# Optimization experiments

Measured on AMD Instinct MI355X. Metric: run time of the kernel, lower is better.

## Reference

```python
import jax, jax.numpy as jnp
import numpy as np

INPUT, HIDDEN, OUT = 512, 512, 1

def setup_inputs() -> dict:
    key = jax.random.key(0)
    ks = jax.random.split(key, 7)
    B, T = 64, 1024
    s_x = 1.0 / np.sqrt(INPUT)
    s_h = 1.0 / np.sqrt(HIDDEN)
    return {
        "x": jax.random.normal(ks[0], (B, T, INPUT), dtype=jnp.float32),
        "W_x": jax.random.uniform(ks[1], (INPUT, HIDDEN), jnp.float32, -s_x, s_x),
        "b_x": jax.random.uniform(ks[2], (HIDDEN,), jnp.float32, -s_x, s_x),
        "W_h": jax.random.uniform(ks[3], (HIDDEN, HIDDEN), jnp.float32, -s_h, s_h),
        "b_h": jax.random.uniform(ks[4], (HIDDEN,), jnp.float32, -s_h, s_h),
        "W_fc": jax.random.uniform(ks[5], (HIDDEN, OUT), jnp.float32, -s_h, s_h),
        "b_fc": jax.random.uniform(ks[6], (OUT,), jnp.float32, -s_h, s_h),
    }

def reference(x, W_x, b_x, W_h, b_h, W_fc, b_fc):
    # Inference mode: dropout is identity (nn.Dropout in eval).
    B = x.shape[0]
    # Precompute input projections for all timesteps in one GEMM: [B,T,H]
    xw = jnp.einsum('bti,ih->bth', x, W_x) + b_x + b_h
    h0 = jnp.zeros((B, HIDDEN), dtype=x.dtype)
    def step(h, xw_t):
        h = jnp.tanh(xw_t + h @ W_h)
        return h, None
    h_T, _ = jax.lax.scan(step, h0, jnp.swapaxes(xw, 0, 1))  # scan over T
    return h_T @ W_fc + b_fc
```

## Files before the change

kernel.cpp:

```cpp
#include <hip/hip_runtime.h>
#include <hip/hip_bf16.h>


#define T_STEPS 1024
#define HID     512

typedef __attribute__((ext_vector_type(8))) short  short8;
typedef __attribute__((ext_vector_type(4))) short  short4_t;
typedef __attribute__((ext_vector_type(4))) float  f32x4;

typedef unsigned short ushort_t;
typedef unsigned int   uint_t;

__device__ __forceinline__ ushort_t f2bf(float f) {
    union { float f; uint_t u; } c; c.f = f;
    uint_t u = c.u;
    return (ushort_t)((u + 0x7fffu + ((u >> 16) & 1u)) >> 16);
}
__device__ __forceinline__ float bf2f(ushort_t h) {
    union { uint_t u; float f; } c; c.u = ((uint_t)h) << 16;
    return c.f;
}
__device__ __forceinline__ float tanh_fast(float x) {
    float t = __builtin_amdgcn_exp2f(x * 2.88539008f);
    return 1.0f - 2.0f * __builtin_amdgcn_rcpf(t + 1.0f);
}

__global__ __launch_bounds__(256) void k1_xproj(
    const float* __restrict__ x, const float* __restrict__ Wx,
    const float* __restrict__ bx, const float* __restrict__ bh,
    ushort_t* __restrict__ xw)
{
    __shared__ __align__(16) ushort_t Wl[64 * 40];
    __shared__ __align__(16) ushort_t Xl[4][64 * 40];

    const int t0   = blockIdx.y * 4;
    const int n0   = blockIdx.x * 64;
    const int tid  = threadIdx.x;
    const int wave = tid >> 6;
    const int lane = tid & 63;
    const int lm   = lane & 15;
    const int quad = lane >> 4;

    f32x4 acc[4][4];
    #pragma unroll
    for (int tt = 0; tt < 4; ++tt)
        #pragma unroll
        for (int i = 0; i < 4; ++i) acc[tt][i] = (f32x4){0.f, 0.f, 0.f, 0.f};

    float biasv[4];
    #pragma unroll
    for (int r = 0; r < 4; ++r) {
        int n = n0 + wave * 16 + quad * 4 + r;
        biasv[r] = bx[n] + bh[n];
    }

    const int ar = tid >> 2, ac = (tid & 3) * 8;
    const int bk = tid >> 3, bc = (tid & 7) * 8;

    for (int kb = 0; kb < 16; ++kb) {
        {
            const float* bp = Wx + (size_t)(kb * 32 + bk) * HID + n0 + bc;
            #pragma unroll
            for (int i = 0; i < 8; ++i) Wl[(bc + i) * 40 + bk] = f2bf(bp[i]);
        }
        #pragma unroll
        for (int tt = 0; tt < 4; ++tt) {
            const float* ap = x + ((size_t)ar * T_STEPS + t0 + tt) * HID + kb * 32 + ac;
            short8 pack;
            #pragma unroll
            for (int i = 0; i < 8; ++i) pack[i] = (short)f2bf(ap[i]);
            *(short8*)&Xl[tt][ar * 40 + ac] = pack;
        }
        __syncthreads();
        short8 afr = *(const short8*)&Wl[(wave * 16 + lm) * 40 + quad * 8];
        #pragma unroll
        for (int tt = 0; tt < 4; ++tt)
            #pragma unroll
            for (int bt = 0; bt < 4; ++bt) {
                short8 bfr = *(const short8*)&Xl[tt][(bt * 16 + lm) * 40 + quad * 8];
                acc[tt][bt] = __builtin_amdgcn_mfma_f32_16x16x32_bf16(afr, bfr, acc[tt][bt], 0, 0, 0);
            }
        __syncthreads();
    }

    #pragma unroll
    for (int tt = 0; tt < 4; ++tt)
        #pragma unroll
        for (int bt = 0; bt < 4; ++bt) {
            short4_t pk;
            #pragma unroll
            for (int r = 0; r < 4; ++r) pk[r] = (short)f2bf(acc[tt][bt][r] + biasv[r]);
            *(short4_t*)&xw[((size_t)(t0 + tt) * 64 + bt * 16 + lm) * HID
                            + n0 + wave * 16 + quad * 4] = pk;
        }
}

__global__ __launch_bounds__(512, 2) void k2_scan(
    const ushort_t* __restrict__ xw, const float* __restrict__ Wh,
    const float* __restrict__ Wfc, const float* __restrict__ bfc,
    float* __restrict__ out)
{
    __shared__ __align__(16) ushort_t hT[2][8192];
    __shared__ __align__(16) ushort_t Wl[49152];

    const int tid  = threadIdx.x;
    const int wave = tid >> 6;
    const int lane = tid & 63;
    const int lm   = lane & 15;
    const int quad = lane >> 4;
    const int rowbase = blockIdx.x * 16;
    const int colb    = wave * 64;

    for (int i = tid; i < 8192; i += 512) hT[0][i] = 0;

    for (int i = 0; i < 12; ++i) {
        int c   = i * 512 + tid;
        int l   = c & 63;
        int mtg = (c >> 6) & 31;
        int ktp = c >> 11;
        int n   = mtg * 16 + (l & 15);
        int kb  = (13 + ktp) * 32 + (l >> 4) * 8;
        short8 w;
        #pragma unroll
        for (int j = 0; j < 8; ++j) w[j] = (short)f2bf(Wh[(size_t)(kb + j) * HID + n]);
        *(short8*)&Wl[(size_t)c * 8] = w;
    }

    short8 wfA[4][13];
    #pragma unroll
    for (int mt = 0; mt < 4; ++mt) {
        const int n = colb + mt * 16 + lm;
        #pragma unroll
        for (int kt = 0; kt < 13; ++kt) {
            short8 w;
            #pragma unroll
            for (int j = 0; j < 8; ++j)
                w[j] = (short)f2bf(Wh[(size_t)(kt * 32 + quad * 8 + j) * HID + n]);
            wfA[mt][kt] = w;
        }
    }
    __syncthreads();

    for (int t = 0; t < T_STEPS; ++t) {
        short4_t xv[4];
        #pragma unroll
        for (int mt = 0; mt < 4; ++mt)
            xv[mt] = *(const short4_t*)&xw[((size_t)t * 64 + rowbase + lm) * HID
                                           + colb + mt * 16 + quad * 4];

        f32x4 acc[4];
        #pragma unroll
        for (int mt = 0; mt < 4; ++mt) acc[mt] = (f32x4){0.f, 0.f, 0.f, 0.f};

        const ushort_t* cur = hT[t & 1];
        #pragma unroll
        for (int kt = 0; kt < 13; ++kt) {
            short8 b = *(const short8*)&cur[(kt * 64 + lane) * 8];
            #pragma unroll
            for (int mt = 0; mt < 4; ++mt)
                acc[mt] = __builtin_amdgcn_mfma_f32_16x16x32_bf16(wfA[mt][kt], b, acc[mt], 0, 0, 0);
        }
        #pragma unroll
        for (int ktp = 0; ktp < 3; ++ktp) {
            short8 b = *(const short8*)&cur[((13 + ktp) * 64 + lane) * 8];
            #pragma unroll
            for (int mt = 0; mt < 4; ++mt) {
                short8 a = *(const short8*)&Wl[(size_t)((ktp * 32 + wave * 4 + mt) * 64 + lane) * 8];
                acc[mt] = __builtin_amdgcn_mfma_f32_16x16x32_bf16(a, b, acc[mt], 0, 0, 0);
            }
        }

        ushort_t* nxt = hT[(t + 1) & 1];
        #pragma unroll
        for (int mt = 0; mt < 4; ++mt) {
            float v0 = tanh_fast(acc[mt][0] + bf2f((ushort_t)xv[mt][0]));
            float v1 = tanh_fast(acc[mt][1] + bf2f((ushort_t)xv[mt][1]));
            float v2 = tanh_fast(acc[mt][2] + bf2f((ushort_t)xv[mt][2]));
            float v3 = tanh_fast(acc[mt][3] + bf2f((ushort_t)xv[mt][3]));
            union { short4_t v; __hip_bfloat162 h[2]; } cv;
            cv.h[0] = __float22bfloat162_rn(float2{v0, v1});
            cv.h[1] = __float22bfloat162_rn(float2{v2, v3});
            const int n = colb + mt * 16 + quad * 4;
            *(short4_t*)&nxt[((n >> 5) * 64 + ((n >> 3) & 3) * 16 + lm) * 8 + (n & 7)] = cv.v;
        }

        __syncthreads();
    }

    const ushort_t* fin = hT[T_STEPS & 1];
    #pragma unroll
    for (int bb = 0; bb < 2; ++bb) {
        const int b = wave * 2 + bb;
        short8 hv = *(const short8*)&fin[(((lane >> 2) * 64 + (lane & 3) * 16 + b) * 8)];
        float s = 0.f;
        #pragma unroll
        for (int j = 0; j < 8; ++j) s += bf2f((ushort_t)hv[j]) * Wfc[lane * 8 + j];
        #pragma unroll
        for (int off = 32; off; off >>= 1) s += __shfl_down(s, off, 64);
        if (lane == 0) out[rowbase + b] = s + bfc[0];
    }
}

extern "C" void kernel_launch(void* const* d_in, const int* in_sizes, int n_in,
                              void* d_out, int out_size, void* d_ws, size_t ws_size,
                              hipStream_t stream)
{
    const float* x   = (const float*)d_in[0];
    const float* Wx  = (const float*)d_in[1];
    const float* bx  = (const float*)d_in[2];
    const float* Wh  = (const float*)d_in[3];
    const float* bh  = (const float*)d_in[4];
    const float* Wfc = (const float*)d_in[5];
    const float* bfc = (const float*)d_in[6];
    float* out = (float*)d_out;

    ushort_t* xw = (ushort_t*)d_ws;

    k1_xproj<<<dim3(8, 256), 256, 0, stream>>>(x, Wx, bx, bh, xw);
    k2_scan <<<dim3(4),      512, 0, stream>>>(xw, Wh, Wfc, bfc, out);
}
```

Baseline: 2.772 ms.

## Widen xproj tiles to 256 columns and shift Wh split toward LDS

The input-projection kernel now uses 512-thread blocks covering 256 output columns and 4 timesteps, so each x tile is loaded and converted once for four times as many columns, and x is read with float4 loads. In the scan kernel, one more K-tile of W_h moves from registers to LDS (12 register tiles instead of 13, 4 LDS tiles instead of 3), which frees VGPRs at the cost of extra LDS reads per step. The xw pointer is also strength-reduced across timesteps. Risks include higher register pressure in k1 (32 accumulators plus 8 A fragments) and more LDS traffic on the serial scan's critical path.

```diff
diff --git a/kernel.cpp b/kernel.cpp
--- a/kernel.cpp
+++ b/kernel.cpp
@@ -8,6 +8,7 @@
 typedef __attribute__((ext_vector_type(8))) short  short8;
 typedef __attribute__((ext_vector_type(4))) short  short4_t;
 typedef __attribute__((ext_vector_type(4))) float  f32x4;
+typedef __attribute__((ext_vector_type(4))) float  float4_t;
 
 typedef unsigned short ushort_t;
 typedef unsigned int   uint_t;
@@ -26,74 +27,80 @@
     return 1.0f - 2.0f * __builtin_amdgcn_rcpf(t + 1.0f);
 }
 
-__global__ __launch_bounds__(256) void k1_xproj(
+__global__ __launch_bounds__(512) void k1_xproj(
     const float* __restrict__ x, const float* __restrict__ Wx,
     const float* __restrict__ bx, const float* __restrict__ bh,
     ushort_t* __restrict__ xw)
 {
-    __shared__ __align__(16) ushort_t Wl[64 * 40];
+    __shared__ __align__(16) ushort_t Wl[256 * 40];
     __shared__ __align__(16) ushort_t Xl[4][64 * 40];
 
-    const int t0   = blockIdx.y * 4;
-    const int n0   = blockIdx.x * 64;
-    const int tid  = threadIdx.x;
-    const int wave = tid >> 6;
-    const int lane = tid & 63;
-    const int lm   = lane & 15;
-    const int quad = lane >> 4;
-
-    f32x4 acc[4][4];
-    #pragma unroll
-    for (int tt = 0; tt < 4; ++tt)
-        #pragma unroll
-        for (int i = 0; i < 4; ++i) acc[tt][i] = (f32x4){0.f, 0.f, 0.f, 0.f};
-
-    float biasv[4];
-    #pragma unroll
-    for (int r = 0; r < 4; ++r) {
-        int n = n0 + wave * 16 + quad * 4 + r;
-        biasv[r] = bx[n] + bh[n];
-    }
-
-    const int ar = tid >> 2, ac = (tid & 3) * 8;
-    const int bk = tid >> 3, bc = (tid & 7) * 8;
+    const int n0    = blockIdx.x * 256;
+    const int t0    = blockIdx.y * 4;
+    const int tid   = threadIdx.x;
+    const int wave  = tid >> 6;
+    const int lane  = tid & 63;
+    const int lm    = lane & 15;
+    const int quad  = lane >> 4;
+    const int t_loc = wave & 3;
+    const int nsub  = (wave >> 2) * 128;
+
+    f32x4 acc[8][4];
+    #pragma unroll
+    for (int mt = 0; mt < 8; ++mt)
+        #pragma unroll
+        for (int bt = 0; bt < 4; ++bt) acc[mt][bt] = (f32x4){0.f, 0.f, 0.f, 0.f};
+
+    const int wk = tid >> 4, wc = (tid & 15) * 16;
+    const int xb = tid >> 3, xc = (tid & 7) * 4;
 
     for (int kb = 0; kb < 16; ++kb) {
         {
-            const float* bp = Wx + (size_t)(kb * 32 + bk) * HID + n0 + bc;
-            #pragma unroll
-            for (int i = 0; i < 8; ++i) Wl[(bc + i) * 40 + bk] = f2bf(bp[i]);
+            const float* wp = Wx + (size_t)(kb * 32 + wk) * HID + n0 + wc;
+            #pragma unroll
+            for (int j = 0; j < 16; ++j) Wl[(wc + j) * 40 + wk] = f2bf(wp[j]);
         }
         #pragma unroll
         for (int tt = 0; tt < 4; ++tt) {
-            const float* ap = x + ((size_t)ar * T_STEPS + t0 + tt) * HID + kb * 32 + ac;
-            short8 pack;
-            #pragma unroll
-            for (int i = 0; i < 8; ++i) pack[i] = (short)f2bf(ap[i]);
-            *(short8*)&Xl[tt][ar * 40 + ac] = pack;
+            const float* ap = x + ((size_t)xb * T_STEPS + t0 + tt) * HID + kb * 32 + xc;
+            float4_t v = *(const float4_t*)ap;
+            short4_t pk;
+            #pragma unroll
+            for (int j = 0; j < 4; ++j) pk[j] = (short)f2bf(v[j]);
+            *(short4_t*)&Xl[tt][xb * 40 + xc] = pk;
         }
         __syncthreads();
-        short8 afr = *(const short8*)&Wl[(wave * 16 + lm) * 40 + quad * 8];
-        #pragma unroll
-        for (int tt = 0; tt < 4; ++tt)
-            #pragma unroll
-            for (int bt = 0; bt < 4; ++bt) {
-                short8 bfr = *(const short8*)&Xl[tt][(bt * 16 + lm) * 40 + quad * 8];
-                acc[tt][bt] = __builtin_amdgcn_mfma_f32_16x16x32_bf16(afr, bfr, acc[tt][bt], 0, 0, 0);
-            }
+        short8 afr[8];
+        #pragma unroll
+        for (int mt = 0; mt < 8; ++mt)
+            afr[mt] = *(const short8*)&Wl[(nsub + mt * 16 + lm) * 40 + quad * 8];
+        #pragma unroll
+        for (int bt = 0; bt < 4; ++bt) {
+            short8 bfr = *(const short8*)&Xl[t_loc][(bt * 16 + lm) * 40 + quad * 8];
+            #pragma unroll
+            for (int mt = 0; mt < 8; ++mt)
+                acc[mt][bt] = __builtin_amdgcn_mfma_f32_16x16x32_bf16(afr[mt], bfr, acc[mt][bt], 0, 0, 0);
+        }
         __syncthreads();
     }
 
     #pragma unroll
-    for (int tt = 0; tt < 4; ++tt)
+    for (int mt = 0; mt < 8; ++mt) {
+        float biasv[4];
+        #pragma unroll
+        for (int r = 0; r < 4; ++r) {
+            int n = n0 + nsub + mt * 16 + quad * 4 + r;
+            biasv[r] = bx[n] + bh[n];
+        }
         #pragma unroll
         for (int bt = 0; bt < 4; ++bt) {
             short4_t pk;
             #pragma unroll
-            for (int r = 0; r < 4; ++r) pk[r] = (short)f2bf(acc[tt][bt][r] + biasv[r]);
-            *(short4_t*)&xw[((size_t)(t0 + tt) * 64 + bt * 16 + lm) * HID
-                            + n0 + wave * 16 + quad * 4] = pk;
-        }
+            for (int r = 0; r < 4; ++r) pk[r] = (short)f2bf(acc[mt][bt][r] + biasv[r]);
+            *(short4_t*)&xw[((size_t)(t0 + t_loc) * 64 + bt * 16 + lm) * HID
+                            + n0 + nsub + mt * 16 + quad * 4] = pk;
+        }
+    }
 }
 
 __global__ __launch_bounds__(512, 2) void k2_scan(
@@ -102,7 +109,7 @@
     float* __restrict__ out)
 {
     __shared__ __align__(16) ushort_t hT[2][8192];
-    __shared__ __align__(16) ushort_t Wl[49152];
+    __shared__ __align__(16) ushort_t Wl[65536];
 
     const int tid  = threadIdx.x;
     const int wave = tid >> 6;
@@ -114,25 +121,25 @@
 
     for (int i = tid; i < 8192; i += 512) hT[0][i] = 0;
 
-    for (int i = 0; i < 12; ++i) {
+    for (int i = 0; i < 16; ++i) {
         int c   = i * 512 + tid;
         int l   = c & 63;
         int mtg = (c >> 6) & 31;
         int ktp = c >> 11;
         int n   = mtg * 16 + (l & 15);
-        int kb  = (13 + ktp) * 32 + (l >> 4) * 8;
+        int kb  = (12 + ktp) * 32 + (l >> 4) * 8;
         short8 w;
         #pragma unroll
         for (int j = 0; j < 8; ++j) w[j] = (short)f2bf(Wh[(size_t)(kb + j) * HID + n]);
         *(short8*)&Wl[(size_t)c * 8] = w;
     }
 
-    short8 wfA[4][13];
+    short8 wfA[4][12];
     #pragma unroll
     for (int mt = 0; mt < 4; ++mt) {
         const int n = colb + mt * 16 + lm;
         #pragma unroll
-        for (int kt = 0; kt < 13; ++kt) {
+        for (int kt = 0; kt < 12; ++kt) {
             short8 w;
             #pragma unroll
             for (int j = 0; j < 8; ++j)
@@ -142,12 +149,13 @@
     }
     __syncthreads();
 
-    for (int t = 0; t < T_STEPS; ++t) {
+    const ushort_t* xp = xw + ((size_t)rowbase + lm) * HID + colb + quad * 4;
+
+    for (int t = 0; t < T_STEPS; ++t, xp += (size_t)64 * HID) {
         short4_t xv[4];
         #pragma unroll
         for (int mt = 0; mt < 4; ++mt)
-            xv[mt] = *(const short4_t*)&xw[((size_t)t * 64 + rowbase + lm) * HID
-                                           + colb + mt * 16 + quad * 4];
+            xv[mt] = *(const short4_t*)(xp + mt * 16);
 
         f32x4 acc[4];
         #pragma unroll
@@ -155,15 +163,15 @@
 
         const ushort_t* cur = hT[t & 1];
         #pragma unroll
-        for (int kt = 0; kt < 13; ++kt) {
+        for (int kt = 0; kt < 12; ++kt) {
             short8 b = *(const short8*)&cur[(kt * 64 + lane) * 8];
             #pragma unroll
             for (int mt = 0; mt < 4; ++mt)
                 acc[mt] = __builtin_amdgcn_mfma_f32_16x16x32_bf16(wfA[mt][kt], b, acc[mt], 0, 0, 0);
         }
         #pragma unroll
-        for (int ktp = 0; ktp < 3; ++ktp) {
-            short8 b = *(const short8*)&cur[((13 + ktp) * 64 + lane) * 8];
+        for (int ktp = 0; ktp < 4; ++ktp) {
+            short8 b = *(const short8*)&cur[((12 + ktp) * 64 + lane) * 8];
             #pragma unroll
             for (int mt = 0; mt < 4; ++mt) {
                 short8 a = *(const short8*)&Wl[(size_t)((ktp * 32 + wave * 4 + mt) * 64 + lane) * 8];
@@ -217,6 +225,6 @@
 
     ushort_t* xw = (ushort_t*)d_ws;
 
-    k1_xproj<<<dim3(8, 256), 256, 0, stream>>>(x, Wx, bx, bh, xw);
+    k1_xproj<<<dim3(2, 256), 512, 0, stream>>>(x, Wx, bx, bh, xw);
     k2_scan <<<dim3(4),      512, 0, stream>>>(xw, Wh, Wfc, bfc, out);
 }
```

Measured after the change: 2.264 ms. -18.3%, faster.
